# Kernel optimization log

Hardware: AMD Instinct MI355X
Metric: run time of the kernel (lower is better)

The kernel has to match this reference:

```python
import jax, jax.numpy as jnp
import numpy as np

B, T, DE, HE, HD = 8192, 128, 6, 512, 512
DT = 0.01


def setup_inputs() -> dict:
    key = jax.random.key(0)
    ks = jax.random.split(key, 10)
    def p(k, shape, s=0.1):
        return jax.random.normal(k, shape, dtype=jnp.float32) * s
    return {
        "e":     jax.random.normal(ks[0], (B, T, DE), dtype=jnp.float32),
        "e_dot": jax.random.normal(ks[1], (B, T, DE), dtype=jnp.float32),
        # EnergyFunction params: fc1 (HE, DE+1), fc2 (1, HE)
        "We1": p(ks[2], (HE, DE + 1)), "be1": p(ks[3], (HE,)),
        "we2": p(ks[4], (1, HE)),      "be2": p(ks[5], (1,)),
        # InverseDissipationPotential params: fc1 (HD, DE+1), fc2 (1, HD)
        "Wd1": p(ks[6], (HD, DE + 1)), "bd1": p(ks[7], (HD,)),
        "wd2": p(ks[8], (1, HD)),      "bd2": p(ks[9], (1,)),
    }


def _mlp_sum(u, v, W1, b1, w2, b2):
    # sum_b [ w2 @ relu(W1 [u;v] + b1)^2 + b2 ]  -- scalar
    x = jnp.concatenate([u, v], axis=-1)          # [B, d_u + d_v]
    h = jax.nn.relu(x @ W1.T + b1)                # [B, H]
    return jnp.sum((h * h) @ w2.T + b2)


def _grads(u, v, W1, b1, w2, b2):
    # (dE/du, dE/dv) of the summed potential == per-sample grads (batch-diagonal)
    return jax.grad(_mlp_sum, argnums=(0, 1))(u, v, W1, b1, w2, b2)


def _forward(e, e_dot, We1, be1, we2, be2, Wd1, bd1, wd2, bd2):
    Bn = e.shape[0]
    xi0 = jnp.zeros((Bn, 1), dtype=e.dtype)
    s_eq0, d0 = _grads(e[:, 0], xi0, We1, be1, we2, be2)
    s_neq0 = jnp.zeros_like(e[:, 0])  # placeholder, overwritten at step 1

    @jax.checkpoint
    def step(carry, inp):
        xi, s_eq, d, _ = carry
        e_i, ed_im1 = inp
        s_neq, kinetics = _grads(ed_im1, -d, Wd1, bd1, wd2, bd2)
        xi_new = xi + DT * kinetics
        stress_i = s_eq - s_neq
        s_eq_new, d_new = _grads(e_i, xi_new, We1, be1, we2, be2)
        return (xi_new, s_eq_new, d_new, s_neq), (stress_i, xi_new)

    e_seq = jnp.swapaxes(e[:, 1:], 0, 1)        # [T-1, B, DE]
    ed_seq = jnp.swapaxes(e_dot[:, :-1], 0, 1)  # [T-1, B, DE]
    (xiT, s_eqT, dT, s_neqT), (stress_seq, xi_seq) = jax.lax.scan(
        step, (xi0, s_eq0, d0, s_neq0), (e_seq, ed_seq))

    last_stress = s_eqT - s_neqT                          # [B, DE]
    stress = jnp.concatenate(
        [jnp.swapaxes(stress_seq, 0, 1), last_stress[:, None]], axis=1)  # [B, T, DE]
    xi = jnp.concatenate(
        [xi0[:, None], jnp.swapaxes(xi_seq, 0, 1)], axis=1)              # [B, T, 1]
    return stress, xi


def reference(e, e_dot, We1, be1, we2, be2, Wd1, bd1, wd2, bd2):
    return _forward(e, e_dot, We1, be1, we2, be2, Wd1, bd1, wd2, bd2)
```

## Files before the change

kernel.cpp:

```cpp
#include <hip/hip_runtime.h>

typedef __attribute__((ext_vector_type(8))) short s8v;
typedef __attribute__((ext_vector_type(4))) float f4v;
typedef __attribute__((ext_vector_type(2))) float f2v;

#define NB 8192
#define NT 128
#define DTC 0.01f

union S8 { s8v v; int i[4]; };
union F4 { f4v v; float f[4]; };

static __device__ __forceinline__ int cvtpk(float lo, float hi) {
    int r;
    asm("v_cvt_pk_bf16_f32 %0, %1, %2" : "=v"(r) : "v"(lo), "v"(hi));
    return r;
}

static __device__ __forceinline__ f4v mfma16(s8v a, s8v b, f4v c) {
    return __builtin_amdgcn_mfma_f32_16x16x32_bf16(a, b, c, 0, 0, 0);
}

static __device__ __forceinline__ void bar_lds() {
    asm volatile("s_waitcnt lgkmcnt(0)\n\ts_barrier" ::: "memory");
}

static __device__ __forceinline__ void volley(const S8* A1m, s8v X, F4* t) {
    const f4v z = {0.f, 0.f, 0.f, 0.f};
#pragma unroll
    for (int tau = 0; tau < 8; ++tau) t[tau].v = mfma16(A1m[tau].v, X, z);
}

static __device__ __forceinline__ void corr8(F4* t, const f4v* w6m, float x6) {
    const f4v sp = {x6, x6, x6, x6};
#pragma unroll
    for (int tau = 0; tau < 8; ++tau)
        t[tau].v = __builtin_elementwise_fma(w6m[tau], sp, t[tau].v);
}

static __device__ __forceinline__ f4v packL2(const S8* A2m, const F4* t) {
    const f4v z = {0.f, 0.f, 0.f, 0.f};
    S8 B[4];
#pragma unroll
    for (int c = 0; c < 4; ++c) {
        f4v r0 = __builtin_elementwise_max(t[2 * c].v, z);
        f4v r1 = __builtin_elementwise_max(t[2 * c + 1].v, z);
        B[c].i[0] = cvtpk(r0.x, r0.y);
        B[c].i[1] = cvtpk(r0.z, r0.w);
        B[c].i[2] = cvtpk(r1.x, r1.y);
        B[c].i[3] = cvtpk(r1.z, r1.w);
    }
    f4v a = mfma16(A2m[0].v, B[0].v, z);
    a = mfma16(A2m[1].v, B[1].v, a);
    f4v b = mfma16(A2m[2].v, B[2].v, z);
    b = mfma16(A2m[3].v, B[3].v, b);
    return a + b;
}

__global__ __launch_bounds__(256, 2)
void visco10(const float* __restrict__ e,
             const float* __restrict__ ed,
             const float* __restrict__ We1,
             const float* __restrict__ be1,
             const float* __restrict__ we2,
             const float* __restrict__ Wd1,
             const float* __restrict__ bd1,
             const float* __restrict__ wd2,
             float* __restrict__ out_s,
             float* __restrict__ out_xi)
{
    __shared__ F4 redS[4][32];
    __shared__ f4v dredD[16], dredE[16];

    const int tid = threadIdx.x;
    const int lane = tid & 63;
    const int w = tid >> 6;
    const int s = lane & 15;
    const int g = lane >> 4;
    const bool g0 = (g == 0);
    const int K67 = 0x3F800000;

    S8 A1[2][8], A2[2][4];
    f4v w6r[2][8];
    {
        const float* W1s[2] = {We1, Wd1};
        const float* b1s[2] = {be1, bd1};
        const float* w2s[2] = {we2, wd2};
#pragma unroll
        for (int p = 0; p < 2; ++p) {
            const float* W1 = W1s[p];
            const float* b1 = b1s[p];
            const float* w2 = w2s[p];
            const float sgn = (p == 1) ? -1.0f : 1.0f;
#pragma unroll
            for (int tau = 0; tau < 8; ++tau) {
                S8 f; f.i[0] = f.i[1] = f.i[2] = f.i[3] = 0;
                if (g0) {
                    const int H = w * 128 + tau * 16 + s;
                    const float* row = W1 + H * 7;
                    f.i[0] = cvtpk(row[0], row[1]);
                    f.i[1] = cvtpk(row[2], row[3]);
                    f.i[2] = cvtpk(row[4], row[5]);
                    f.i[3] = cvtpk(row[6], b1[H]);
                }
                A1[p][tau] = f;
                const int Hj = w * 128 + tau * 16 + 4 * g;
                f4v wv;
                wv.x = sgn * W1[(Hj + 0) * 7 + 6];
                wv.y = sgn * W1[(Hj + 1) * 7 + 6];
                wv.z = sgn * W1[(Hj + 2) * 7 + 6];
                wv.w = sgn * W1[(Hj + 3) * 7 + 6];
                w6r[p][tau] = wv;
            }
#pragma unroll
            for (int c = 0; c < 4; ++c) {
                S8 f;
#pragma unroll
                for (int ii = 0; ii < 4; ++ii) {
                    const int i0 = 2 * ii, i1 = 2 * ii + 1;
                    const int H0 = w * 128 + (2 * c + (i0 >> 2)) * 16 + 4 * g + (i0 & 3);
                    const int H1 = w * 128 + (2 * c + (i1 >> 2)) * 16 + 4 * g + (i1 & 3);
                    const float v0 = (s < 7) ? W1[H0 * 7 + s] * 2.0f * w2[H0] : 0.f;
                    const float v1 = (s < 7) ? W1[H1 * 7 + s] * 2.0f * w2[H1] : 0.f;
                    f.i[ii] = cvtpk(v0, v1);
                }
                A2[p][c] = f;
            }
        }
    }

    const size_t sm = (size_t)blockIdx.x * 16 + s;
    const f2v* pE = (const f2v*)(e + sm * 768);
    const f2v* pD = (const f2v*)(ed + sm * 768);
    float* sB = out_s + sm * 768;
    float* xB = out_xi + sm * NT;

    f2v p0 = pE[0], p1 = pE[1], p2 = pE[2];
    f2v q0 = pD[0], q1 = pD[1], q2 = pD[2];
    f2v eR0 = pE[3], eR1 = pE[4], eR2 = pE[5];
    f2v dR0 = pD[3], dR1 = pD[4], dR2 = pD[5];

    F4 t[8];
    S8 X;
    F4 accD, accE;

    X.i[0] = g0 ? cvtpk(p0.x, p0.y) : 0;
    X.i[1] = g0 ? cvtpk(p1.x, p1.y) : 0;
    X.i[2] = g0 ? cvtpk(p2.x, p2.y) : 0;
    X.i[3] = g0 ? K67 : 0;
    volley(A1[0], X.v, t);
    accE.v = packL2(A2[0], t);
    if (g == 1) ((float*)&dredE[s])[w] = accE.f[2];
    int xd0 = cvtpk(q0.x, q0.y), xd1 = cvtpk(q1.x, q1.y), xd2 = cvtpk(q2.x, q2.y);
    int xe0 = 0, xe1 = 0, xe2 = 0;
    float xi = 0.f;
    if (w == 1 && g0) xB[0] = 0.f;

#pragma unroll 1
    for (int it = 0; it < NT - 1; ++it) {
        bar_lds();
        F4 dp; dp.v = dredE[s];
        X.i[0] = g0 ? xd0 : 0;
        X.i[1] = g0 ? xd1 : 0;
        X.i[2] = g0 ? xd2 : 0;
        X.i[3] = g0 ? K67 : 0;
        volley(A1[1], X.v, t);
        const float d = (dp.f[0] + dp.f[1]) + (dp.f[2] + dp.f[3]);
        corr8(t, w6r[1], d);
        accD.v = packL2(A2[1], t);
        F4 sp; sp.v = accE.v - accD.v;
        if (lane < 32) redS[w][lane].v = sp.v;
        if (g == 1) ((float*)&dredD[s])[w] = accD.f[2];
        xe0 = cvtpk(eR0.x, eR0.y); xe1 = cvtpk(eR1.x, eR1.y); xe2 = cvtpk(eR2.x, eR2.y);
        {
            const int tn = (it + 2 < NT) ? it + 2 : NT - 1;
            eR0 = pE[3 * tn]; eR1 = pE[3 * tn + 1]; eR2 = pE[3 * tn + 2];
        }

        bar_lds();
        F4 dq; dq.v = dredD[s];
        X.i[0] = g0 ? xe0 : 0;
        X.i[1] = g0 ? xe1 : 0;
        X.i[2] = g0 ? xe2 : 0;
        X.i[3] = g0 ? K67 : 0;
        volley(A1[0], X.v, t);
        if (w == 3) {
            const int l31 = lane & 31;
            f4v st = (redS[0][l31].v + redS[1][l31].v) +
                     (redS[2][l31].v + redS[3][l31].v);
            float* ps = sB + it * 6;
            if (g == 0) {
                ((f2v*)ps)[0] = f2v{st.x, st.y};
                ((f2v*)ps)[1] = f2v{st.z, st.w};
            } else if (g == 1) {
                ((f2v*)ps)[2] = f2v{st.x, st.y};
            }
        }
        const float kin = (dq.f[0] + dq.f[1]) + (dq.f[2] + dq.f[3]);
        xi = fmaf(DTC, kin, xi);
        if (w == 1 && g0) xB[it + 1] = xi;
        corr8(t, w6r[0], xi);
        accE.v = packL2(A2[0], t);
        if (g == 1) ((float*)&dredE[s])[w] = accE.f[2];
        xd0 = cvtpk(dR0.x, dR0.y); xd1 = cvtpk(dR1.x, dR1.y); xd2 = cvtpk(dR2.x, dR2.y);
        {
            const int tn = (it + 2 < NT) ? it + 2 : NT - 1;
            dR0 = pD[3 * tn]; dR1 = pD[3 * tn + 1]; dR2 = pD[3 * tn + 2];
        }
    }

    bar_lds();
    F4 spf; spf.v = accE.v - accD.v;
    if (lane < 32) redS[w][lane].v = spf.v;
    bar_lds();
    if (w == 3) {
        const int l31 = lane & 31;
        f4v st = (redS[0][l31].v + redS[1][l31].v) +
                 (redS[2][l31].v + redS[3][l31].v);
        float* ps = sB + (NT - 1) * 6;
        if (g == 0) {
            ((f2v*)ps)[0] = f2v{st.x, st.y};
            ((f2v*)ps)[1] = f2v{st.z, st.w};
        } else if (g == 1) {
            ((f2v*)ps)[2] = f2v{st.x, st.y};
        }
    }
}

extern "C" void kernel_launch(void* const* d_in, const int* in_sizes, int n_in,
                              void* d_out, int out_size, void* d_ws, size_t ws_size,
                              hipStream_t stream) {
    const float* e    = (const float*)d_in[0];
    const float* edot = (const float*)d_in[1];
    const float* We1  = (const float*)d_in[2];
    const float* be1  = (const float*)d_in[3];
    const float* we2  = (const float*)d_in[4];
    const float* Wd1  = (const float*)d_in[6];
    const float* bd1  = (const float*)d_in[7];
    const float* wd2  = (const float*)d_in[8];

    float* out_stress = (float*)d_out;
    float* out_xi     = (float*)d_out + (size_t)NB * NT * 6;

    visco10<<<NB / 16, 256, 0, stream>>>(e, edot, We1, be1, we2,
                                         Wd1, bd1, wd2, out_stress, out_xi);
}
```

Before: 162.1 us.

## Split hidden units across eight waves and stage layer-2 weights in LDS

Doubles the block to 512 threads so each wave owns 64 hidden units instead of 128. This halves the per-wave MFMA chain in each recurrent step and doubles the waves available to hide latency. To fit the register budget, the layer-2 fragments and xi/d column weights move to shared memory and are reloaded each step. The cross-wave reductions grow to eight partials. The stress store alternates between two waves. The trade-off is extra LDS traffic and wider barriers on every step.

```diff
diff --git a/kernel.cpp b/kernel.cpp
--- a/kernel.cpp
+++ b/kernel.cpp
@@ -1,4 +1,5 @@
 #include <hip/hip_runtime.h>
+
 
 typedef __attribute__((ext_vector_type(8))) short s8v;
 typedef __attribute__((ext_vector_type(4))) float f4v;
@@ -25,40 +26,45 @@
     asm volatile("s_waitcnt lgkmcnt(0)\n\ts_barrier" ::: "memory");
 }
 
-static __device__ __forceinline__ void volley(const S8* A1m, s8v X, F4* t) {
+static __device__ __forceinline__ void volley4(const S8* A1m, s8v X, F4* t) {
     const f4v z = {0.f, 0.f, 0.f, 0.f};
 #pragma unroll
-    for (int tau = 0; tau < 8; ++tau) t[tau].v = mfma16(A1m[tau].v, X, z);
-}
-
-static __device__ __forceinline__ void corr8(F4* t, const f4v* w6m, float x6) {
+    for (int tau = 0; tau < 4; ++tau) t[tau].v = mfma16(A1m[tau].v, X, z);
+}
+
+static __device__ __forceinline__ void corr4(F4* t, const f4v* w6t, float x6) {
     const f4v sp = {x6, x6, x6, x6};
 #pragma unroll
-    for (int tau = 0; tau < 8; ++tau)
-        t[tau].v = __builtin_elementwise_fma(w6m[tau], sp, t[tau].v);
-}
-
-static __device__ __forceinline__ f4v packL2(const S8* A2m, const F4* t) {
+    for (int tau = 0; tau < 4; ++tau)
+        t[tau].v = __builtin_elementwise_fma(w6t[tau], sp, t[tau].v);
+}
+
+static __device__ __forceinline__ f4v packL2_2(s8v a20, s8v a21, const F4* t) {
     const f4v z = {0.f, 0.f, 0.f, 0.f};
-    S8 B[4];
-#pragma unroll
-    for (int c = 0; c < 4; ++c) {
-        f4v r0 = __builtin_elementwise_max(t[2 * c].v, z);
-        f4v r1 = __builtin_elementwise_max(t[2 * c + 1].v, z);
-        B[c].i[0] = cvtpk(r0.x, r0.y);
-        B[c].i[1] = cvtpk(r0.z, r0.w);
-        B[c].i[2] = cvtpk(r1.x, r1.y);
-        B[c].i[3] = cvtpk(r1.z, r1.w);
-    }
-    f4v a = mfma16(A2m[0].v, B[0].v, z);
-    a = mfma16(A2m[1].v, B[1].v, a);
-    f4v b = mfma16(A2m[2].v, B[2].v, z);
-    b = mfma16(A2m[3].v, B[3].v, b);
+    S8 B0, B1;
+    {
+        f4v r0 = __builtin_elementwise_max(t[0].v, z);
+        f4v r1 = __builtin_elementwise_max(t[1].v, z);
+        B0.i[0] = cvtpk(r0.x, r0.y);
+        B0.i[1] = cvtpk(r0.z, r0.w);
+        B0.i[2] = cvtpk(r1.x, r1.y);
+        B0.i[3] = cvtpk(r1.z, r1.w);
+    }
+    {
+        f4v r2 = __builtin_elementwise_max(t[2].v, z);
+        f4v r3 = __builtin_elementwise_max(t[3].v, z);
+        B1.i[0] = cvtpk(r2.x, r2.y);
+        B1.i[1] = cvtpk(r2.z, r2.w);
+        B1.i[2] = cvtpk(r3.x, r3.y);
+        B1.i[3] = cvtpk(r3.z, r3.w);
+    }
+    f4v a = mfma16(a20, B0.v, z);
+    f4v b = mfma16(a21, B1.v, z);
     return a + b;
 }
 
-__global__ __launch_bounds__(256, 2)
-void visco10(const float* __restrict__ e,
+__global__ __launch_bounds__(512, 4)
+void visco11(const float* __restrict__ e,
              const float* __restrict__ ed,
              const float* __restrict__ We1,
              const float* __restrict__ be1,
@@ -69,8 +75,11 @@
              float* __restrict__ out_s,
              float* __restrict__ out_xi)
 {
-    __shared__ F4 redS[4][32];
-    __shared__ f4v dredD[16], dredE[16];
+    __shared__ F4 redS[8][32];
+    __shared__ __align__(16) float dredD[16][12];
+    __shared__ __align__(16) float dredE[16][12];
+    __shared__ f4v w6lds[2][128];
+    __shared__ s8v a2lds[2][8][2][64];
 
     const int tid = threadIdx.x;
     const int lane = tid & 63;
@@ -80,8 +89,7 @@
     const bool g0 = (g == 0);
     const int K67 = 0x3F800000;
 
-    S8 A1[2][8], A2[2][4];
-    f4v w6r[2][8];
+    S8 A1[2][4];
     {
         const float* W1s[2] = {We1, Wd1};
         const float* b1s[2] = {be1, bd1};
@@ -92,11 +100,15 @@
             const float* b1 = b1s[p];
             const float* w2 = w2s[p];
             const float sgn = (p == 1) ? -1.0f : 1.0f;
-#pragma unroll
-            for (int tau = 0; tau < 8; ++tau) {
+            {
+                const int H = w * 64 + lane;
+                ((float*)&w6lds[p][0])[H] = sgn * W1[H * 7 + 6];
+            }
+#pragma unroll
+            for (int tau = 0; tau < 4; ++tau) {
                 S8 f; f.i[0] = f.i[1] = f.i[2] = f.i[3] = 0;
                 if (g0) {
-                    const int H = w * 128 + tau * 16 + s;
+                    const int H = w * 64 + tau * 16 + s;
                     const float* row = W1 + H * 7;
                     f.i[0] = cvtpk(row[0], row[1]);
                     f.i[1] = cvtpk(row[2], row[3]);
@@ -104,30 +116,24 @@
                     f.i[3] = cvtpk(row[6], b1[H]);
                 }
                 A1[p][tau] = f;
-                const int Hj = w * 128 + tau * 16 + 4 * g;
-                f4v wv;
-                wv.x = sgn * W1[(Hj + 0) * 7 + 6];
-                wv.y = sgn * W1[(Hj + 1) * 7 + 6];
-                wv.z = sgn * W1[(Hj + 2) * 7 + 6];
-                wv.w = sgn * W1[(Hj + 3) * 7 + 6];
-                w6r[p][tau] = wv;
-            }
-#pragma unroll
-            for (int c = 0; c < 4; ++c) {
+            }
+#pragma unroll
+            for (int c = 0; c < 2; ++c) {
                 S8 f;
 #pragma unroll
                 for (int ii = 0; ii < 4; ++ii) {
                     const int i0 = 2 * ii, i1 = 2 * ii + 1;
-                    const int H0 = w * 128 + (2 * c + (i0 >> 2)) * 16 + 4 * g + (i0 & 3);
-                    const int H1 = w * 128 + (2 * c + (i1 >> 2)) * 16 + 4 * g + (i1 & 3);
+                    const int H0 = w * 64 + (2 * c + (i0 >> 2)) * 16 + 4 * g + (i0 & 3);
+                    const int H1 = w * 64 + (2 * c + (i1 >> 2)) * 16 + 4 * g + (i1 & 3);
                     const float v0 = (s < 7) ? W1[H0 * 7 + s] * 2.0f * w2[H0] : 0.f;
                     const float v1 = (s < 7) ? W1[H1 * 7 + s] * 2.0f * w2[H1] : 0.f;
                     f.i[ii] = cvtpk(v0, v1);
                 }
-                A2[p][c] = f;
-            }
-        }
-    }
+                a2lds[p][w][c][lane] = f.v;
+            }
+        }
+    }
+    bar_lds();
 
     const size_t sm = (size_t)blockIdx.x * 16 + s;
     const f2v* pE = (const f2v*)(e + sm * 768);
@@ -140,54 +146,74 @@
     f2v eR0 = pE[3], eR1 = pE[4], eR2 = pE[5];
     f2v dR0 = pD[3], dR1 = pD[4], dR2 = pD[5];
 
-    F4 t[8];
-    S8 X;
+    F4 t[4];
+    S8 XD, XE;
     F4 accD, accE;
-
-    X.i[0] = g0 ? cvtpk(p0.x, p0.y) : 0;
-    X.i[1] = g0 ? cvtpk(p1.x, p1.y) : 0;
-    X.i[2] = g0 ? cvtpk(p2.x, p2.y) : 0;
-    X.i[3] = g0 ? K67 : 0;
-    volley(A1[0], X.v, t);
-    accE.v = packL2(A2[0], t);
-    if (g == 1) ((float*)&dredE[s])[w] = accE.f[2];
-    int xd0 = cvtpk(q0.x, q0.y), xd1 = cvtpk(q1.x, q1.y), xd2 = cvtpk(q2.x, q2.y);
-    int xe0 = 0, xe1 = 0, xe2 = 0;
+    XD.i[3] = K67;
+    XE.i[3] = K67;
+
+    XE.i[0] = cvtpk(p0.x, p0.y);
+    XE.i[1] = cvtpk(p1.x, p1.y);
+    XE.i[2] = cvtpk(p2.x, p2.y);
+    volley4(A1[0], XE.v, t);
+    {
+        S8 a20, a21;
+        a20.v = a2lds[0][w][0][lane];
+        a21.v = a2lds[0][w][1][lane];
+        accE.v = packL2_2(a20.v, a21.v, t);
+    }
+    if (g == 1) dredE[s][w] = accE.f[2];
+    XD.i[0] = cvtpk(q0.x, q0.y);
+    XD.i[1] = cvtpk(q1.x, q1.y);
+    XD.i[2] = cvtpk(q2.x, q2.y);
     float xi = 0.f;
     if (w == 1 && g0) xB[0] = 0.f;
 
 #pragma unroll 1
     for (int it = 0; it < NT - 1; ++it) {
         bar_lds();
-        F4 dp; dp.v = dredE[s];
-        X.i[0] = g0 ? xd0 : 0;
-        X.i[1] = g0 ? xd1 : 0;
-        X.i[2] = g0 ? xd2 : 0;
-        X.i[3] = g0 ? K67 : 0;
-        volley(A1[1], X.v, t);
-        const float d = (dp.f[0] + dp.f[1]) + (dp.f[2] + dp.f[3]);
-        corr8(t, w6r[1], d);
-        accD.v = packL2(A2[1], t);
+        F4 dpA, dpB;
+        dpA.v = *(const f4v*)&dredE[s][0];
+        dpB.v = *(const f4v*)&dredE[s][4];
+        f4v w6t[4];
+#pragma unroll
+        for (int tau = 0; tau < 4; ++tau) w6t[tau] = w6lds[1][w * 16 + tau * 4 + g];
+        S8 a20, a21;
+        a20.v = a2lds[1][w][0][lane];
+        a21.v = a2lds[1][w][1][lane];
+        volley4(A1[1], XD.v, t);
+        F4 dsm; dsm.v = dpA.v + dpB.v;
+        const float d = (dsm.f[0] + dsm.f[1]) + (dsm.f[2] + dsm.f[3]);
+        corr4(t, w6t, d);
+        accD.v = packL2_2(a20.v, a21.v, t);
         F4 sp; sp.v = accE.v - accD.v;
         if (lane < 32) redS[w][lane].v = sp.v;
-        if (g == 1) ((float*)&dredD[s])[w] = accD.f[2];
-        xe0 = cvtpk(eR0.x, eR0.y); xe1 = cvtpk(eR1.x, eR1.y); xe2 = cvtpk(eR2.x, eR2.y);
+        if (g == 1) dredD[s][w] = accD.f[2];
+        XE.i[0] = cvtpk(eR0.x, eR0.y);
+        XE.i[1] = cvtpk(eR1.x, eR1.y);
+        XE.i[2] = cvtpk(eR2.x, eR2.y);
         {
             const int tn = (it + 2 < NT) ? it + 2 : NT - 1;
             eR0 = pE[3 * tn]; eR1 = pE[3 * tn + 1]; eR2 = pE[3 * tn + 2];
         }
 
         bar_lds();
-        F4 dq; dq.v = dredD[s];
-        X.i[0] = g0 ? xe0 : 0;
-        X.i[1] = g0 ? xe1 : 0;
-        X.i[2] = g0 ? xe2 : 0;
-        X.i[3] = g0 ? K67 : 0;
-        volley(A1[0], X.v, t);
-        if (w == 3) {
+        F4 dqA, dqB;
+        dqA.v = *(const f4v*)&dredD[s][0];
+        dqB.v = *(const f4v*)&dredD[s][4];
+        f4v w6u[4];
+#pragma unroll
+        for (int tau = 0; tau < 4; ++tau) w6u[tau] = w6lds[0][w * 16 + tau * 4 + g];
+        S8 b20, b21;
+        b20.v = a2lds[0][w][0][lane];
+        b21.v = a2lds[0][w][1][lane];
+        volley4(A1[0], XE.v, t);
+        if (w == 6 + (it & 1)) {
             const int l31 = lane & 31;
-            f4v st = (redS[0][l31].v + redS[1][l31].v) +
-                     (redS[2][l31].v + redS[3][l31].v);
+            f4v st = ((redS[0][l31].v + redS[1][l31].v) +
+                      (redS[2][l31].v + redS[3][l31].v)) +
+                     ((redS[4][l31].v + redS[5][l31].v) +
+                      (redS[6][l31].v + redS[7][l31].v));
             float* ps = sB + it * 6;
             if (g == 0) {
                 ((f2v*)ps)[0] = f2v{st.x, st.y};
@@ -196,13 +222,16 @@
                 ((f2v*)ps)[2] = f2v{st.x, st.y};
             }
         }
+        F4 dq; dq.v = dqA.v + dqB.v;
         const float kin = (dq.f[0] + dq.f[1]) + (dq.f[2] + dq.f[3]);
         xi = fmaf(DTC, kin, xi);
         if (w == 1 && g0) xB[it + 1] = xi;
-        corr8(t, w6r[0], xi);
-        accE.v = packL2(A2[0], t);
-        if (g == 1) ((float*)&dredE[s])[w] = accE.f[2];
-        xd0 = cvtpk(dR0.x, dR0.y); xd1 = cvtpk(dR1.x, dR1.y); xd2 = cvtpk(dR2.x, dR2.y);
+        corr4(t, w6u, xi);
+        accE.v = packL2_2(b20.v, b21.v, t);
+        if (g == 1) dredE[s][w] = accE.f[2];
+        XD.i[0] = cvtpk(dR0.x, dR0.y);
+        XD.i[1] = cvtpk(dR1.x, dR1.y);
+        XD.i[2] = cvtpk(dR2.x, dR2.y);
         {
             const int tn = (it + 2 < NT) ? it + 2 : NT - 1;
             dR0 = pD[3 * tn]; dR1 = pD[3 * tn + 1]; dR2 = pD[3 * tn + 2];
@@ -213,10 +242,12 @@
     F4 spf; spf.v = accE.v - accD.v;
     if (lane < 32) redS[w][lane].v = spf.v;
     bar_lds();
-    if (w == 3) {
+    if (w == 7) {
         const int l31 = lane & 31;
-        f4v st = (redS[0][l31].v + redS[1][l31].v) +
-                 (redS[2][l31].v + redS[3][l31].v);
+        f4v st = ((redS[0][l31].v + redS[1][l31].v) +
+                  (redS[2][l31].v + redS[3][l31].v)) +
+                 ((redS[4][l31].v + redS[5][l31].v) +
+                  (redS[6][l31].v + redS[7][l31].v));
         float* ps = sB + (NT - 1) * 6;
         if (g == 0) {
             ((f2v*)ps)[0] = f2v{st.x, st.y};
@@ -242,6 +273,6 @@
     float* out_stress = (float*)d_out;
     float* out_xi     = (float*)d_out + (size_t)NB * NT * 6;
 
-    visco10<<<NB / 16, 256, 0, stream>>>(e, edot, We1, be1, we2,
+    visco11<<<NB / 16, 512, 0, stream>>>(e, edot, We1, be1, we2,
                                          Wd1, bd1, wd2, out_stress, out_xi);
 }
```

Result: slower. 355.5 us (+119.3%).

## Issue next-phase MFMA volleys early to overlap with dependent corrections

Applied to the files above, without the earlier changes.

The layer-1 MFMA volley for each potential depends only on the input (e or e_dot), not on the scalar correction from the other potential. The loop now issues the energy volley before the dissipation correction and pack, and the dissipation volley before the energy correction, using separate accumulator sets. This takes the volleys off the serial dependency chain between barriers so they overlap the LDS reduction latency. It doubles the live accumulator registers, which at launch bounds of 2 blocks per CU risks spills. The stress store wave also alternates between waves 2 and 3 to spread that work.

```diff
diff --git a/kernel.cpp b/kernel.cpp
--- a/kernel.cpp
+++ b/kernel.cpp
@@ -1,4 +1,5 @@
 #include <hip/hip_runtime.h>
+
 
 typedef __attribute__((ext_vector_type(8))) short s8v;
 typedef __attribute__((ext_vector_type(4))) float f4v;
@@ -58,7 +59,7 @@
 }
 
 __global__ __launch_bounds__(256, 2)
-void visco10(const float* __restrict__ e,
+void visco15(const float* __restrict__ e,
              const float* __restrict__ ed,
              const float* __restrict__ We1,
              const float* __restrict__ be1,
@@ -140,19 +141,22 @@
     f2v eR0 = pE[3], eR1 = pE[4], eR2 = pE[5];
     f2v dR0 = pD[3], dR1 = pD[4], dR2 = pD[5];
 
-    F4 t[8];
-    S8 X;
+    F4 tD[8], tE[8];
+    S8 XD, XE;
     F4 accD, accE;
 
-    X.i[0] = g0 ? cvtpk(p0.x, p0.y) : 0;
-    X.i[1] = g0 ? cvtpk(p1.x, p1.y) : 0;
-    X.i[2] = g0 ? cvtpk(p2.x, p2.y) : 0;
-    X.i[3] = g0 ? K67 : 0;
-    volley(A1[0], X.v, t);
-    accE.v = packL2(A2[0], t);
+    XE.i[0] = g0 ? cvtpk(p0.x, p0.y) : 0;
+    XE.i[1] = g0 ? cvtpk(p1.x, p1.y) : 0;
+    XE.i[2] = g0 ? cvtpk(p2.x, p2.y) : 0;
+    XE.i[3] = g0 ? K67 : 0;
+    volley(A1[0], XE.v, tE);
+    accE.v = packL2(A2[0], tE);
     if (g == 1) ((float*)&dredE[s])[w] = accE.f[2];
-    int xd0 = cvtpk(q0.x, q0.y), xd1 = cvtpk(q1.x, q1.y), xd2 = cvtpk(q2.x, q2.y);
-    int xe0 = 0, xe1 = 0, xe2 = 0;
+    XD.i[0] = g0 ? cvtpk(q0.x, q0.y) : 0;
+    XD.i[1] = g0 ? cvtpk(q1.x, q1.y) : 0;
+    XD.i[2] = g0 ? cvtpk(q2.x, q2.y) : 0;
+    XD.i[3] = g0 ? K67 : 0;
+    volley(A1[1], XD.v, tD);
     float xi = 0.f;
     if (w == 1 && g0) xB[0] = 0.f;
 
@@ -160,18 +164,17 @@
     for (int it = 0; it < NT - 1; ++it) {
         bar_lds();
         F4 dp; dp.v = dredE[s];
-        X.i[0] = g0 ? xd0 : 0;
-        X.i[1] = g0 ? xd1 : 0;
-        X.i[2] = g0 ? xd2 : 0;
-        X.i[3] = g0 ? K67 : 0;
-        volley(A1[1], X.v, t);
+        XE.i[0] = g0 ? cvtpk(eR0.x, eR0.y) : 0;
+        XE.i[1] = g0 ? cvtpk(eR1.x, eR1.y) : 0;
+        XE.i[2] = g0 ? cvtpk(eR2.x, eR2.y) : 0;
+        XE.i[3] = g0 ? K67 : 0;
+        volley(A1[0], XE.v, tE);
         const float d = (dp.f[0] + dp.f[1]) + (dp.f[2] + dp.f[3]);
-        corr8(t, w6r[1], d);
-        accD.v = packL2(A2[1], t);
+        corr8(tD, w6r[1], d);
+        accD.v = packL2(A2[1], tD);
         F4 sp; sp.v = accE.v - accD.v;
         if (lane < 32) redS[w][lane].v = sp.v;
         if (g == 1) ((float*)&dredD[s])[w] = accD.f[2];
-        xe0 = cvtpk(eR0.x, eR0.y); xe1 = cvtpk(eR1.x, eR1.y); xe2 = cvtpk(eR2.x, eR2.y);
         {
             const int tn = (it + 2 < NT) ? it + 2 : NT - 1;
             eR0 = pE[3 * tn]; eR1 = pE[3 * tn + 1]; eR2 = pE[3 * tn + 2];
@@ -179,12 +182,12 @@
 
         bar_lds();
         F4 dq; dq.v = dredD[s];
-        X.i[0] = g0 ? xe0 : 0;
-        X.i[1] = g0 ? xe1 : 0;
-        X.i[2] = g0 ? xe2 : 0;
-        X.i[3] = g0 ? K67 : 0;
-        volley(A1[0], X.v, t);
-        if (w == 3) {
+        XD.i[0] = g0 ? cvtpk(dR0.x, dR0.y) : 0;
+        XD.i[1] = g0 ? cvtpk(dR1.x, dR1.y) : 0;
+        XD.i[2] = g0 ? cvtpk(dR2.x, dR2.y) : 0;
+        XD.i[3] = g0 ? K67 : 0;
+        volley(A1[1], XD.v, tD);
+        if (w == 2 + (it & 1)) {
             const int l31 = lane & 31;
             f4v st = (redS[0][l31].v + redS[1][l31].v) +
                      (redS[2][l31].v + redS[3][l31].v);
@@ -199,10 +202,9 @@
         const float kin = (dq.f[0] + dq.f[1]) + (dq.f[2] + dq.f[3]);
         xi = fmaf(DTC, kin, xi);
         if (w == 1 && g0) xB[it + 1] = xi;
-        corr8(t, w6r[0], xi);
-        accE.v = packL2(A2[0], t);
+        corr8(tE, w6r[0], xi);
+        accE.v = packL2(A2[0], tE);
         if (g == 1) ((float*)&dredE[s])[w] = accE.f[2];
-        xd0 = cvtpk(dR0.x, dR0.y); xd1 = cvtpk(dR1.x, dR1.y); xd2 = cvtpk(dR2.x, dR2.y);
         {
             const int tn = (it + 2 < NT) ? it + 2 : NT - 1;
             dR0 = pD[3 * tn]; dR1 = pD[3 * tn + 1]; dR2 = pD[3 * tn + 2];
@@ -242,6 +244,6 @@
     float* out_stress = (float*)d_out;
     float* out_xi     = (float*)d_out + (size_t)NB * NT * 6;
 
-    visco10<<<NB / 16, 256, 0, stream>>>(e, edot, We1, be1, we2,
+    visco15<<<NB / 16, 256, 0, stream>>>(e, edot, We1, be1, we2,
                                          Wd1, bd1, wd2, out_stress, out_xi);
 }
```

After: 246.3 us. 1.52x slower.
